# Performance work log

Measured on AMD Instinct MI355X. Metric: run time of the kernel, lower is better.

The kernel has to match this reference:

```python
import jax, jax.numpy as jnp
import numpy as np

BINS = 10

def setup_inputs() -> dict:
    key = jax.random.key(0)
    k1, k2 = jax.random.split(key)
    N, C = 131072, 1000
    pred = jax.random.normal(k1, (N, C), dtype=jnp.float32)
    target = jax.random.randint(k2, (N,), 0, C, dtype=jnp.int64)
    return {"pred": pred, "target": target}


def reference(pred, target):
    # edges = [0, 0.1, ..., 1.0]; last edge nudged so values_clip == 1.0 lands in last bin
    edges = jnp.arange(BINS + 1, dtype=pred.dtype) / BINS
    edges = edges.at[-1].add(1e-6)

    N = pred.shape[0]
    # per-sample cross entropy: -log_softmax(pred)[i, target[i]]
    log_probs = jax.nn.log_softmax(pred, axis=-1)          # [N, C]
    values = -jnp.take_along_axis(log_probs, target[:, None], axis=-1)[:, 0]  # [N]

    # detached, normalized gradient-magnitude proxy in [0, 1]
    values_clip = jax.lax.stop_gradient(values)
    values_clip = values_clip / jnp.max(values_clip)

    # histogram binning: inds = (vc >= edges[i]) & (vc < edges[i+1])
    bin_idx = jnp.searchsorted(edges, values_clip, side='right') - 1
    bin_idx = jnp.clip(bin_idx, 0, BINS - 1)
    counts = jnp.zeros((BINS,), dtype=pred.dtype).at[bin_idx].add(1.0)

    n_nonempty = jnp.sum(counts > 0).astype(pred.dtype)
    tot = jnp.asarray(N, dtype=pred.dtype)

    # weight per bin = tot / num_in_bin for occupied bins (empty bins never indexed)
    per_bin_w = tot / jnp.where(counts > 0, counts, 1.0)
    weights = per_bin_w[bin_idx] / jnp.maximum(n_nonempty, 1.0) / tot
    weights = jax.lax.stop_gradient(weights)

    return jnp.sum(weights * values)
```

## Files before the change

kernel.cpp:

```cpp
#include <hip/hip_runtime.h>

#define N_SAMPLES 131072
#define N_CLASSES 1000
#define BINS 10


__global__ __launch_bounds__(256) void values_kernel(const float* __restrict__ pred,
                                                     const int* __restrict__ target,
                                                     float* __restrict__ values) {
    const int wave = threadIdx.x >> 6;
    const int lane = threadIdx.x & 63;
    const int row = blockIdx.x * 4 + wave;
    if (row >= N_SAMPLES) return;

    const float4* __restrict__ rp = (const float4*)(pred + (size_t)row * N_CLASSES);

    float4 r[4];
    float lmax = -INFINITY;
#pragma unroll
    for (int k = 0; k < 4; ++k) {
        int idx = k * 64 + lane;
        if (idx < 250) {
            r[k] = rp[idx];
            lmax = fmaxf(lmax, fmaxf(fmaxf(r[k].x, r[k].y), fmaxf(r[k].z, r[k].w)));
        }
    }
#pragma unroll
    for (int off = 32; off > 0; off >>= 1)
        lmax = fmaxf(lmax, __shfl_xor(lmax, off, 64));

    float s = 0.f;
#pragma unroll
    for (int k = 0; k < 4; ++k) {
        int idx = k * 64 + lane;
        if (idx < 250) {
            s += __expf(r[k].x - lmax);
            s += __expf(r[k].y - lmax);
            s += __expf(r[k].z - lmax);
            s += __expf(r[k].w - lmax);
        }
    }
#pragma unroll
    for (int off = 32; off > 0; off >>= 1)
        s += __shfl_xor(s, off, 64);

    if (lane == 0) {
        float xt = pred[(size_t)row * N_CLASSES + target[row]];
        values[row] = logf(s) + lmax - xt;
    }
}

__global__ __launch_bounds__(256) void max_kernel(const float* __restrict__ values,
                                                  unsigned int* __restrict__ vmax_bits) {
    __shared__ float smax[4];
    float m = 0.f;
    for (int i = blockIdx.x * blockDim.x + threadIdx.x; i < N_SAMPLES;
         i += gridDim.x * blockDim.x)
        m = fmaxf(m, values[i]);
#pragma unroll
    for (int off = 32; off > 0; off >>= 1)
        m = fmaxf(m, __shfl_xor(m, off, 64));
    if ((threadIdx.x & 63) == 0) smax[threadIdx.x >> 6] = m;
    __syncthreads();
    if (threadIdx.x == 0) {
        float bm = fmaxf(fmaxf(smax[0], smax[1]), fmaxf(smax[2], smax[3]));
        atomicMax(vmax_bits, __float_as_uint(bm));
    }
}

__global__ __launch_bounds__(256) void hist_kernel(const float* __restrict__ values,
                                                   const unsigned int* __restrict__ vmax_bits,
                                                   unsigned int* __restrict__ counts,
                                                   float* __restrict__ sums) {
    __shared__ unsigned int lc[BINS];
    __shared__ float ls[BINS];
    if (threadIdx.x < BINS) { lc[threadIdx.x] = 0u; ls[threadIdx.x] = 0.f; }
    __syncthreads();

    const float vmax = __uint_as_float(*vmax_bits);
    float edges[BINS + 1];
#pragma unroll
    for (int j = 0; j <= BINS; ++j) edges[j] = (float)j / 10.0f;
    edges[BINS] += 1e-6f;

    for (int i = blockIdx.x * blockDim.x + threadIdx.x; i < N_SAMPLES;
         i += gridDim.x * blockDim.x) {
        float v = values[i];
        float vc = v / vmax;
        int bin = -1;
#pragma unroll
        for (int j = 0; j <= BINS; ++j) bin += (edges[j] <= vc) ? 1 : 0;
        bin = min(max(bin, 0), BINS - 1);
        atomicAdd(&lc[bin], 1u);
        atomicAdd(&ls[bin], v);
    }
    __syncthreads();
    if (threadIdx.x < BINS) {
        if (lc[threadIdx.x]) {
            atomicAdd(&counts[threadIdx.x], lc[threadIdx.x]);
            atomicAdd(&sums[threadIdx.x], ls[threadIdx.x]);
        }
    }
}

__global__ void final_kernel(const unsigned int* __restrict__ counts,
                             const float* __restrict__ sums,
                             float* __restrict__ out) {
    if (threadIdx.x == 0 && blockIdx.x == 0) {
        int nn = 0;
        float acc = 0.f;
#pragma unroll
        for (int b = 0; b < BINS; ++b) {
            unsigned int c = counts[b];
            if (c > 0u) { ++nn; acc += sums[b] / (float)c; }
        }
        float nne = (nn > 0) ? (float)nn : 1.f;
        out[0] = acc / nne;
    }
}

extern "C" void kernel_launch(void* const* d_in, const int* in_sizes, int n_in,
                              void* d_out, int out_size, void* d_ws, size_t ws_size,
                              hipStream_t stream) {
    const float* pred = (const float*)d_in[0];
    const int* target = (const int*)d_in[1];
    float* out = (float*)d_out;

    float* values = (float*)d_ws;
    unsigned int* stats = (unsigned int*)((char*)d_ws + (size_t)N_SAMPLES * sizeof(float));
    unsigned int* counts = stats + 1;
    float* sums = (float*)(stats + 11);

    hipMemsetAsync(stats, 0, 21 * sizeof(unsigned int), stream);

    values_kernel<<<N_SAMPLES / 4, 256, 0, stream>>>(pred, target, values);
    max_kernel<<<256, 256, 0, stream>>>(values, stats);
    hist_kernel<<<256, 256, 0, stream>>>(values, stats, counts, sums);
    final_kernel<<<1, 64, 0, stream>>>(counts, sums, out);
}
```

Baseline: 670.6 us.

## Fuse max into values kernel and merge histogram with final reduction

The global max reduction now happens inside the per-row cross-entropy kernel through a block-level max and an atomicMax. The histogram and final combine run as one 1024-thread single-block kernel that keeps cumulative threshold counts and sums in registers, so it needs no per-element atomics. This drops two kernel launches and the extra pass over the values array. The cost is that the histogram runs on a single block, and cumulative float counts and differenced sums could differ slightly from exact per-bin values.

```diff
diff --git a/kernel.cpp b/kernel.cpp
--- a/kernel.cpp
+++ b/kernel.cpp
@@ -5,13 +5,14 @@
 #define BINS 10
 
 
-__global__ __launch_bounds__(256) void values_kernel(const float* __restrict__ pred,
-                                                     const int* __restrict__ target,
-                                                     float* __restrict__ values) {
+__global__ __launch_bounds__(256) void values_max_kernel(const float* __restrict__ pred,
+                                                         const int* __restrict__ target,
+                                                         float* __restrict__ values,
+                                                         unsigned int* __restrict__ vmax_bits) {
+    __shared__ float smax[4];
     const int wave = threadIdx.x >> 6;
     const int lane = threadIdx.x & 63;
-    const int row = blockIdx.x * 4 + wave;
-    if (row >= N_SAMPLES) return;
+    const int row  = blockIdx.x * 4 + wave;
 
     const float4* __restrict__ rp = (const float4*)(pred + (size_t)row * N_CLASSES);
 
@@ -44,23 +45,13 @@
     for (int off = 32; off > 0; off >>= 1)
         s += __shfl_xor(s, off, 64);
 
+    float v = 0.f;
     if (lane == 0) {
         float xt = pred[(size_t)row * N_CLASSES + target[row]];
-        values[row] = logf(s) + lmax - xt;
+        v = logf(s) + lmax - xt;
+        values[row] = v;
+        smax[wave] = v;
     }
-}
-
-__global__ __launch_bounds__(256) void max_kernel(const float* __restrict__ values,
-                                                  unsigned int* __restrict__ vmax_bits) {
-    __shared__ float smax[4];
-    float m = 0.f;
-    for (int i = blockIdx.x * blockDim.x + threadIdx.x; i < N_SAMPLES;
-         i += gridDim.x * blockDim.x)
-        m = fmaxf(m, values[i]);
-#pragma unroll
-    for (int off = 32; off > 0; off >>= 1)
-        m = fmaxf(m, __shfl_xor(m, off, 64));
-    if ((threadIdx.x & 63) == 0) smax[threadIdx.x >> 6] = m;
     __syncthreads();
     if (threadIdx.x == 0) {
         float bm = fmaxf(fmaxf(smax[0], smax[1]), fmaxf(smax[2], smax[3]));
@@ -68,51 +59,83 @@
     }
 }
 
-__global__ __launch_bounds__(256) void hist_kernel(const float* __restrict__ values,
-                                                   const unsigned int* __restrict__ vmax_bits,
-                                                   unsigned int* __restrict__ counts,
-                                                   float* __restrict__ sums) {
-    __shared__ unsigned int lc[BINS];
-    __shared__ float ls[BINS];
-    if (threadIdx.x < BINS) { lc[threadIdx.x] = 0u; ls[threadIdx.x] = 0.f; }
+__global__ __launch_bounds__(1024) void hist_final_kernel(const float* __restrict__ values,
+                                                          const unsigned int* __restrict__ vmax_bits,
+                                                          float* __restrict__ out) {
+    __shared__ float scum[BINS];
+    __shared__ float scs[BINS + 1];
+    const int tid  = threadIdx.x;
+    const int lane = tid & 63;
+    const int wv   = tid >> 6;
+
+    if (tid < BINS) scum[tid] = 0.f;
+    if (tid < BINS + 1) scs[tid] = 0.f;
     __syncthreads();
 
     const float vmax = __uint_as_float(*vmax_bits);
-    float edges[BINS + 1];
+    const float inv  = 1.0f / vmax;
+
+    float edge[9];
 #pragma unroll
-    for (int j = 0; j <= BINS; ++j) edges[j] = (float)j / 10.0f;
-    edges[BINS] += 1e-6f;
+    for (int j = 0; j < 9; ++j) edge[j] = (float)(j + 1) / 10.0f;
 
-    for (int i = blockIdx.x * blockDim.x + threadIdx.x; i < N_SAMPLES;
-         i += gridDim.x * blockDim.x) {
-        float v = values[i];
-        float vc = v / vmax;
-        int bin = -1;
+    float cum[9];
+    float cs[10];
 #pragma unroll
-        for (int j = 0; j <= BINS; ++j) bin += (edges[j] <= vc) ? 1 : 0;
-        bin = min(max(bin, 0), BINS - 1);
-        atomicAdd(&lc[bin], 1u);
-        atomicAdd(&ls[bin], v);
+    for (int j = 0; j < 9; ++j) cum[j] = 0.f;
+#pragma unroll
+    for (int j = 0; j < 10; ++j) cs[j] = 0.f;
+
+    const float4* __restrict__ vp = (const float4*)values;
+#pragma unroll 4
+    for (int k = 0; k < N_SAMPLES / 4 / 1024; ++k) {
+        float4 v4 = vp[tid + 1024 * k];
+        float vv[4] = {v4.x, v4.y, v4.z, v4.w};
+#pragma unroll
+        for (int c = 0; c < 4; ++c) {
+            float v  = vv[c];
+            float vc = v * inv;
+            cs[0] += v;
+#pragma unroll
+            for (int j = 0; j < 9; ++j) {
+                bool m = (vc >= edge[j]);
+                cum[j] += m ? 1.f : 0.f;
+                cs[j + 1] += m ? v : 0.f;
+            }
+        }
+    }
+
+#pragma unroll
+    for (int off = 32; off > 0; off >>= 1) {
+#pragma unroll
+        for (int j = 0; j < 9; ++j) cum[j] += __shfl_xor(cum[j], off, 64);
+#pragma unroll
+        for (int j = 0; j < 10; ++j) cs[j] += __shfl_xor(cs[j], off, 64);
+    }
+    if (lane == 0) {
+        (void)wv;
+#pragma unroll
+        for (int j = 0; j < 9; ++j) atomicAdd(&scum[j], cum[j]);
+#pragma unroll
+        for (int j = 0; j < 10; ++j) atomicAdd(&scs[j], cs[j]);
     }
     __syncthreads();
-    if (threadIdx.x < BINS) {
-        if (lc[threadIdx.x]) {
-            atomicAdd(&counts[threadIdx.x], lc[threadIdx.x]);
-            atomicAdd(&sums[threadIdx.x], ls[threadIdx.x]);
-        }
-    }
-}
 
-__global__ void final_kernel(const unsigned int* __restrict__ counts,
-                             const float* __restrict__ sums,
-                             float* __restrict__ out) {
-    if (threadIdx.x == 0 && blockIdx.x == 0) {
+    if (tid == 0) {
+        float c_edge[11], s_edge[11];
+        c_edge[0] = (float)N_SAMPLES;
+        s_edge[0] = scs[0];
+#pragma unroll
+        for (int j = 1; j <= 9; ++j) { c_edge[j] = scum[j - 1]; s_edge[j] = scs[j]; }
+        c_edge[10] = 0.f; s_edge[10] = 0.f;
+
         int nn = 0;
         float acc = 0.f;
 #pragma unroll
         for (int b = 0; b < BINS; ++b) {
-            unsigned int c = counts[b];
-            if (c > 0u) { ++nn; acc += sums[b] / (float)c; }
+            float cb = c_edge[b] - c_edge[b + 1];
+            float sb = s_edge[b] - s_edge[b + 1];
+            if (cb > 0.5f) { ++nn; acc += sb / cb; }
         }
         float nne = (nn > 0) ? (float)nn : 1.f;
         out[0] = acc / nne;
@@ -122,19 +145,14 @@
 extern "C" void kernel_launch(void* const* d_in, const int* in_sizes, int n_in,
                               void* d_out, int out_size, void* d_ws, size_t ws_size,
                               hipStream_t stream) {
-    const float* pred = (const float*)d_in[0];
-    const int* target = (const int*)d_in[1];
-    float* out = (float*)d_out;
+    const float* pred  = (const float*)d_in[0];
+    const int* target  = (const int*)d_in[1];
+    float* out         = (float*)d_out;
 
-    float* values = (float*)d_ws;
-    unsigned int* stats = (unsigned int*)((char*)d_ws + (size_t)N_SAMPLES * sizeof(float));
-    unsigned int* counts = stats + 1;
-    float* sums = (float*)(stats + 11);
+    float* values           = (float*)d_ws;
+    unsigned int* vmax_bits = (unsigned int*)((char*)d_ws + (size_t)N_SAMPLES * sizeof(float));
 
-    hipMemsetAsync(stats, 0, 21 * sizeof(unsigned int), stream);
-
-    values_kernel<<<N_SAMPLES / 4, 256, 0, stream>>>(pred, target, values);
-    max_kernel<<<256, 256, 0, stream>>>(values, stats);
-    hist_kernel<<<256, 256, 0, stream>>>(values, stats, counts, sums);
-    final_kernel<<<1, 64, 0, stream>>>(counts, sums, out);
+    hipMemsetAsync(vmax_bits, 0, sizeof(unsigned int), stream);
+    values_max_kernel<<<N_SAMPLES / 4, 256, 0, stream>>>(pred, target, values, vmax_bits);
+    hist_final_kernel<<<1, 1024, 0, stream>>>(values, vmax_bits, out);
 }
```

Measured after the change: 943.9 us. 40.8% more time.
